# Kernel optimization log

Measured on AMD Instinct MI355X. Metric: run time of the kernel, lower is better.

The kernel has to match this reference:

```python
import jax, jax.numpy as jnp
import numpy as np

B, D, H, W, K = 32, 64, 32, 32, 8192
BETA, EMA_DECAY, EMA_EPS = 0.25, 0.99, 1e-05


def setup_inputs() -> dict:
    key = jax.random.key(0)
    k1, k2 = jax.random.split(key, 2)
    z = jax.random.normal(k1, (B, D, H, W), dtype=jnp.float32)
    embedding = jax.random.normal(k2, (K, D), dtype=jnp.float32)  # weight.data.normal_()
    ema_cluster_size = jnp.zeros((K,), dtype=jnp.float32)
    ema_embedding_avg = embedding  # initialized as clone of weights
    return {
        "z": z,
        "embedding": embedding,
        "ema_cluster_size": ema_cluster_size,
        "ema_embedding_avg": ema_embedding_avg,
    }


def reference(z, embedding, ema_cluster_size, ema_embedding_avg):
    b, d, h, w = z.shape
    k = embedding.shape[0]
    n = b * h * w

    # (b d h w) -> (b h w) d
    z_flat = jnp.transpose(z, (0, 2, 3, 1)).reshape(n, d)

    # squared L2 distances: ||z||^2 + ||e||^2 - 2 z e^T   -> [n, k]
    distances = (
        jnp.sum(z_flat * z_flat, axis=1, keepdims=True)
        + jnp.sum(embedding * embedding, axis=1)
        - 2.0 * jnp.einsum("nd,kd->nk", z_flat, embedding)
    )
    encoding_indices = jnp.argmin(distances, axis=1)  # [n]

    # codebook gather
    z_q_flat = embedding[encoding_indices]  # [n, d]
    z_quantized = jnp.transpose(z_q_flat.reshape(b, h, w, d), (0, 3, 1, 2))

    # commitment loss (encoder loss; quantized is detached in original)
    loss = BETA * jnp.mean((jax.lax.stop_gradient(z_quantized) - z) ** 2)

    # perplexity from one-hot mean (computed via scatter-add instead of dense one-hot)
    counts = jnp.zeros((k,), dtype=jnp.float32).at[encoding_indices].add(1.0)  # [k]
    enc_mean = counts / n
    perplexity = jnp.exp(-jnp.sum(enc_mean * jnp.log(enc_mean + 1e-10)))

    # EMA codebook update (training path)
    batch_cluster_size = counts
    batch_embedding_avg = jnp.zeros((k, d), dtype=z_flat.dtype).at[encoding_indices].add(z_flat)
    new_cluster_size = EMA_DECAY * ema_cluster_size + (1.0 - EMA_DECAY) * batch_cluster_size
    new_embedding_avg = EMA_DECAY * ema_embedding_avg + (1.0 - EMA_DECAY) * batch_embedding_avg
    new_embedding = new_embedding_avg / (new_cluster_size + EMA_EPS)[:, None]

    # straight-through estimator
    z_quantized_st = z + jax.lax.stop_gradient(z_quantized - z)

    return (
        z_quantized_st,
        loss,
        perplexity,
        encoding_indices,
        new_embedding,
        new_cluster_size,
        new_embedding_avg,
    )
```

## Files before the change

kernel.cpp:

```cpp
#include <hip/hip_runtime.h>
#include <math.h>

#define KCL   8192
#define DIM   64
#define NPTS  32768
#define HW    1024
#define PLANE 65536

__global__ __launch_bounds__(256) void e2_kernel(const float* __restrict__ emb,
                                                 float* __restrict__ e2) {
    int k = blockIdx.x * 256 + threadIdx.x;
    const float4* row = (const float4*)(emb + (size_t)k * DIM);
    float s = 0.f;
#pragma unroll
    for (int i = 0; i < DIM / 4; ++i) {
        float4 v = row[i];
        s += v.x * v.x + v.y * v.y + v.z * v.z + v.w * v.w;
    }
    e2[k] = s;
}

__global__ __launch_bounds__(256) void vq_main(
    const float* __restrict__ z, const float* __restrict__ emb,
    const float* __restrict__ e2g, float* __restrict__ counts,
    float* __restrict__ bavg, float* __restrict__ loss_ws,
    float* __restrict__ zq_out, float* __restrict__ idx_out) {
    __shared__ float z_lds[64 * 68];
    __shared__ float e_lds[64 * 68];
    __shared__ float e2_lds[64];

    const int t   = threadIdx.x;
    const int pg  = t >> 4;
    const int cg  = t & 15;
    const int p0  = blockIdx.x * 64;
    const int b   = p0 >> 10;
    const int hw0 = p0 & 1023;
    const float* zb = z + (size_t)b * PLANE + hw0;

    {
        int seg = t & 15, d0 = t >> 4;
#pragma unroll
        for (int r = 0; r < 4; ++r) {
            int d = d0 + 16 * r;
            float4 v = *(const float4*)(zb + d * HW + 4 * seg);
            *(float4*)&z_lds[d * 68 + 4 * seg] = v;
        }
    }

    float best[4];
    int   bestk[4];
#pragma unroll
    for (int i = 0; i < 4; ++i) { best[i] = 3.4e38f; bestk[i] = 0; }

    for (int k0 = 0; k0 < KCL; k0 += 64) {
        __syncthreads();
        {
            int c = t >> 2, s0 = t & 3;
#pragma unroll
            for (int r = 0; r < 4; ++r) {
                int seg = s0 + 4 * r;
                float4 v = *(const float4*)(emb + (size_t)(k0 + c) * DIM + 4 * seg);
                e_lds[(4 * seg + 0) * 68 + c] = v.x;
                e_lds[(4 * seg + 1) * 68 + c] = v.y;
                e_lds[(4 * seg + 2) * 68 + c] = v.z;
                e_lds[(4 * seg + 3) * 68 + c] = v.w;
            }
            if (t < 64) e2_lds[t] = e2g[k0 + t];
        }
        __syncthreads();

        float acc[4][4];
#pragma unroll
        for (int i = 0; i < 4; ++i)
#pragma unroll
            for (int j = 0; j < 4; ++j) acc[i][j] = 0.f;

#pragma unroll 4
        for (int d = 0; d < 64; ++d) {
            float4 zv = *(const float4*)&z_lds[d * 68 + 4 * pg];
            float4 ev = *(const float4*)&e_lds[d * 68 + 4 * cg];
            acc[0][0] += zv.x * ev.x; acc[0][1] += zv.x * ev.y;
            acc[0][2] += zv.x * ev.z; acc[0][3] += zv.x * ev.w;
            acc[1][0] += zv.y * ev.x; acc[1][1] += zv.y * ev.y;
            acc[1][2] += zv.y * ev.z; acc[1][3] += zv.y * ev.w;
            acc[2][0] += zv.z * ev.x; acc[2][1] += zv.z * ev.y;
            acc[2][2] += zv.z * ev.z; acc[2][3] += zv.z * ev.w;
            acc[3][0] += zv.w * ev.x; acc[3][1] += zv.w * ev.y;
            acc[3][2] += zv.w * ev.z; acc[3][3] += zv.w * ev.w;
        }

#pragma unroll
        for (int i = 0; i < 4; ++i) {
#pragma unroll
            for (int j = 0; j < 4; ++j) {
                float dist = e2_lds[4 * cg + j] - 2.f * acc[i][j];
                int   kk   = k0 + 4 * cg + j;
                if (dist < best[i]) { best[i] = dist; bestk[i] = kk; }
            }
        }
    }

#pragma unroll
    for (int i = 0; i < 4; ++i) {
        float bd = best[i];
        int   bk = bestk[i];
        for (int off = 8; off > 0; off >>= 1) {
            float od = __shfl_xor(bd, off, 16);
            int   ok = __shfl_xor(bk, off, 16);
            if (od < bd || (od == bd && ok < bk)) { bd = od; bk = ok; }
        }
        best[i] = bd; bestk[i] = bk;
    }

    __syncthreads();
    float* zq_lds = e_lds;

    float lsum = 0.f;
#pragma unroll
    for (int j = 0; j < 4; ++j) {
        int k = bestk[j];
        int p = 4 * pg + j;
        float4 ev = *(const float4*)(emb + (size_t)k * DIM + 4 * cg);
        float zv0 = z_lds[(4 * cg + 0) * 68 + p];
        float zv1 = z_lds[(4 * cg + 1) * 68 + p];
        float zv2 = z_lds[(4 * cg + 2) * 68 + p];
        float zv3 = z_lds[(4 * cg + 3) * 68 + p];
        zq_lds[(4 * cg + 0) * 68 + p] = ev.x;
        zq_lds[(4 * cg + 1) * 68 + p] = ev.y;
        zq_lds[(4 * cg + 2) * 68 + p] = ev.z;
        zq_lds[(4 * cg + 3) * 68 + p] = ev.w;
        float d0 = ev.x - zv0, d1 = ev.y - zv1, d2 = ev.z - zv2, d3 = ev.w - zv3;
        lsum += d0 * d0 + d1 * d1 + d2 * d2 + d3 * d3;
        atomicAdd(&bavg[(size_t)k * DIM + 4 * cg + 0], zv0);
        atomicAdd(&bavg[(size_t)k * DIM + 4 * cg + 1], zv1);
        atomicAdd(&bavg[(size_t)k * DIM + 4 * cg + 2], zv2);
        atomicAdd(&bavg[(size_t)k * DIM + 4 * cg + 3], zv3);
        if (cg == 0) {
            atomicAdd(&counts[k], 1.0f);
            idx_out[p0 + p] = (float)k;
        }
    }

#pragma unroll
    for (int off = 32; off > 0; off >>= 1) lsum += __shfl_xor(lsum, off, 64);
    if ((t & 63) == 0) atomicAdd(loss_ws, lsum);

    __syncthreads();
    {
        int seg = t & 15, d0 = t >> 4;
#pragma unroll
        for (int r = 0; r < 4; ++r) {
            int d = d0 + 16 * r;
            float4 q = *(const float4*)&zq_lds[d * 68 + 4 * seg];
            *(float4*)(zq_out + (size_t)b * PLANE + d * HW + hw0 + 4 * seg) = q;
        }
    }
}

__global__ __launch_bounds__(256) void ema_kernel(
    const float* __restrict__ ema_cs, const float* __restrict__ ema_avg,
    const float* __restrict__ counts, const float* __restrict__ bavg,
    float* __restrict__ out_ncs, float* __restrict__ out_navg,
    float* __restrict__ out_nemb) {
    int tid = blockIdx.x * 256 + threadIdx.x;
    int k = tid >> 4;
    float ncs = 0.99f * ema_cs[k] + 0.01f * counts[k];
    float den = ncs + 1e-5f;
    float4 ea = ((const float4*)ema_avg)[tid];
    float4 ba = ((const float4*)bavg)[tid];
    float4 na, ne;
    na.x = 0.99f * ea.x + 0.01f * ba.x;
    na.y = 0.99f * ea.y + 0.01f * ba.y;
    na.z = 0.99f * ea.z + 0.01f * ba.z;
    na.w = 0.99f * ea.w + 0.01f * ba.w;
    ne.x = na.x / den; ne.y = na.y / den; ne.z = na.z / den; ne.w = na.w / den;
    ((float4*)out_navg)[tid] = na;
    ((float4*)out_nemb)[tid] = ne;
    if ((tid & 15) == 0) out_ncs[k] = ncs;
}

__global__ __launch_bounds__(256) void scalars_kernel(
    const float* __restrict__ counts, const float* __restrict__ loss_ws,
    float* __restrict__ out_loss, float* __restrict__ out_perp) {
    __shared__ float red[4];
    float s = 0.f;
    for (int k = threadIdx.x; k < KCL; k += 256) {
        float p = counts[k] * (1.0f / (float)NPTS);
        s += p * logf(p + 1e-10f);
    }
#pragma unroll
    for (int off = 32; off > 0; off >>= 1) s += __shfl_xor(s, off, 64);
    if ((threadIdx.x & 63) == 0) red[threadIdx.x >> 6] = s;
    __syncthreads();
    if (threadIdx.x == 0) {
        float tot = red[0] + red[1] + red[2] + red[3];
        out_perp[0] = expf(-tot);
        out_loss[0] = 0.25f * loss_ws[0] / (float)(NPTS * DIM);
    }
}

extern "C" void kernel_launch(void* const* d_in, const int* in_sizes, int n_in,
                              void* d_out, int out_size, void* d_ws, size_t ws_size,
                              hipStream_t stream) {
    (void)in_sizes; (void)n_in; (void)out_size; (void)ws_size;
    const float* z       = (const float*)d_in[0];
    const float* emb     = (const float*)d_in[1];
    const float* ema_cs  = (const float*)d_in[2];
    const float* ema_avg = (const float*)d_in[3];

    float* out0      = (float*)d_out;
    float* out_loss  = out0 + 2097152;
    float* out_perp  = out_loss + 1;
    float* out_idx   = out_perp + 1;
    float* out_nemb  = out_idx + NPTS;
    float* out_ncs   = out_nemb + KCL * DIM;
    float* out_navg  = out_ncs + KCL;

    float* e2_ws     = (float*)d_ws;
    float* counts_ws = e2_ws + KCL;
    float* bavg_ws   = counts_ws + KCL;
    float* loss_ws   = bavg_ws + KCL * DIM;

    hipMemsetAsync((void*)counts_ws, 0, (size_t)(KCL + KCL * DIM + 1) * sizeof(float), stream);

    e2_kernel<<<KCL / 256, 256, 0, stream>>>(emb, e2_ws);
    vq_main<<<NPTS / 64, 256, 0, stream>>>(z, emb, e2_ws, counts_ws, bavg_ws,
                                           loss_ws, out0, out_idx);
    ema_kernel<<<KCL * DIM / 4 / 256, 256, 0, stream>>>(ema_cs, ema_avg, counts_ws,
                                                        bavg_ws, out_ncs, out_navg, out_nemb);
    scalars_kernel<<<1, 256, 0, stream>>>(counts_ws, loss_ws, out_loss, out_perp);
}
```

Before: 610.6 us.

## Restructure VQ distance loop with double-buffered codebook chunks and wave-level argmin

Reworks the main VQ kernel so each wave owns 16 points, with z read directly from global memory (wave-uniform, cached) and codebook chunks of 128 entries held in a swizzled, double-buffered LDS. The next chunk is prefetched into registers while the current one is computed, leaving one barrier per chunk. Each lane covers 2 codes by 16 points, and the argmin reduces across the full wave. The epilogue is rewritten to gather from global memory per point, and launch bounds request 2 blocks per CU. The risks are higher register pressure from 32 accumulators plus prefetch registers, and repeated global z loads inside the inner loop.

Result: slower. 884.5 us (+44.9%).

```diff
diff --git a/kernel.cpp b/kernel.cpp
--- a/kernel.cpp
+++ b/kernel.cpp
@@ -6,6 +6,10 @@
 #define NPTS  32768
 #define HW    1024
 #define PLANE 65536
+#define CCH   128
+#define NCH   (KCL/CCH)
+#define TP    16
+#define TC    2
 
 __global__ __launch_bounds__(256) void e2_kernel(const float* __restrict__ emb,
                                                  float* __restrict__ e2) {
@@ -20,140 +24,147 @@
     e2[k] = s;
 }
 
-__global__ __launch_bounds__(256) void vq_main(
+#define FMA4(zz, ib) \
+    acc[ib+0][0]=fmaf(zz.x,e0,acc[ib+0][0]); acc[ib+0][1]=fmaf(zz.x,e1,acc[ib+0][1]); \
+    acc[ib+1][0]=fmaf(zz.y,e0,acc[ib+1][0]); acc[ib+1][1]=fmaf(zz.y,e1,acc[ib+1][1]); \
+    acc[ib+2][0]=fmaf(zz.z,e0,acc[ib+2][0]); acc[ib+2][1]=fmaf(zz.z,e1,acc[ib+2][1]); \
+    acc[ib+3][0]=fmaf(zz.w,e0,acc[ib+3][0]); acc[ib+3][1]=fmaf(zz.w,e1,acc[ib+3][1]);
+
+__global__ __launch_bounds__(256, 2) void vq_main(
     const float* __restrict__ z, const float* __restrict__ emb,
     const float* __restrict__ e2g, float* __restrict__ counts,
     float* __restrict__ bavg, float* __restrict__ loss_ws,
     float* __restrict__ zq_out, float* __restrict__ idx_out) {
-    __shared__ float z_lds[64 * 68];
-    __shared__ float e_lds[64 * 68];
-    __shared__ float e2_lds[64];
-
-    const int t   = threadIdx.x;
-    const int pg  = t >> 4;
-    const int cg  = t & 15;
-    const int p0  = blockIdx.x * 64;
-    const int b   = p0 >> 10;
-    const int hw0 = p0 & 1023;
-    const float* zb = z + (size_t)b * PLANE + hw0;
+
+    __shared__ __align__(16) float ebuf[2][CCH * DIM];
+    __shared__ float e2buf[2][CCH];
+    __shared__ int   kbest_lds[64];
+
+    const int t    = threadIdx.x;
+    const int lane = t & 63;
+    const int wuni = __builtin_amdgcn_readfirstlane(t >> 6);
+    const int p0   = blockIdx.x * 64;
+    const int b    = p0 >> 10;
+    const int hw0  = p0 & 1023;
+
+    const float* zw = z + (size_t)b * PLANE + hw0 + 16 * wuni;
+
+    const int srow  = t >> 1;
+    const int sbase = (t & 1) * 8;
+    const int skey  = (t >> 3) & 15;
+    const int rb0 = (2 * lane) * DIM;
+    const int rb1 = rb0 + DIM;
+    const int sw4 = ((lane >> 1) & 15) << 2;
 
     {
-        int seg = t & 15, d0 = t >> 4;
-#pragma unroll
-        for (int r = 0; r < 4; ++r) {
-            int d = d0 + 16 * r;
-            float4 v = *(const float4*)(zb + d * HW + 4 * seg);
-            *(float4*)&z_lds[d * 68 + 4 * seg] = v;
-        }
-    }
-
-    float best[4];
-    int   bestk[4];
-#pragma unroll
-    for (int i = 0; i < 4; ++i) { best[i] = 3.4e38f; bestk[i] = 0; }
-
-    for (int k0 = 0; k0 < KCL; k0 += 64) {
-        __syncthreads();
-        {
-            int c = t >> 2, s0 = t & 3;
-#pragma unroll
-            for (int r = 0; r < 4; ++r) {
-                int seg = s0 + 4 * r;
-                float4 v = *(const float4*)(emb + (size_t)(k0 + c) * DIM + 4 * seg);
-                e_lds[(4 * seg + 0) * 68 + c] = v.x;
-                e_lds[(4 * seg + 1) * 68 + c] = v.y;
-                e_lds[(4 * seg + 2) * 68 + c] = v.z;
-                e_lds[(4 * seg + 3) * 68 + c] = v.w;
+        const float* src = emb + (size_t)srow * DIM;
+#pragma unroll
+        for (int i = 0; i < 8; ++i) {
+            int slot = sbase + i;
+            float4 v = *(const float4*)(src + slot * 4);
+            *(float4*)&ebuf[0][srow * DIM + ((slot ^ skey) << 2)] = v;
+        }
+        e2buf[0][t & 127] = e2g[t & 127];
+    }
+
+    float best[TP]; int bestk[TP];
+#pragma unroll
+    for (int i = 0; i < TP; ++i) { best[i] = 3.4e38f; bestk[i] = 0; }
+
+    __syncthreads();
+
+    for (int kc = 0; kc < NCH; ++kc) {
+        const int cur = kc & 1;
+        const int k0  = kc * CCH;
+
+        float4 st[8]; float e2st = 0.f;
+        const bool more = (kc + 1 < NCH);
+        if (more) {
+            const float* src = emb + (size_t)(k0 + CCH + srow) * DIM;
+#pragma unroll
+            for (int i = 0; i < 8; ++i) st[i] = *(const float4*)(src + (sbase + i) * 4);
+            e2st = e2g[k0 + CCH + (t & 127)];
+        }
+
+        float acc[TP][TC];
+#pragma unroll
+        for (int i = 0; i < TP; ++i) { acc[i][0] = 0.f; acc[i][1] = 0.f; }
+
+        const float* eb = &ebuf[cur][0];
+#pragma unroll 4
+        for (int dg = 0; dg < 16; ++dg) {
+            float4 ea = *(const float4*)&eb[rb0 + ((dg << 2) ^ sw4)];
+            float4 ec = *(const float4*)&eb[rb1 + ((dg << 2) ^ sw4)];
+#pragma unroll
+            for (int dd = 0; dd < 4; ++dd) {
+                const float* zd = zw + (size_t)(4 * dg + dd) * HW;
+                float4 z0 = *(const float4*)(zd);
+                float4 z1 = *(const float4*)(zd + 4);
+                float4 z2 = *(const float4*)(zd + 8);
+                float4 z3 = *(const float4*)(zd + 12);
+                float e0 = (dd == 0) ? ea.x : (dd == 1) ? ea.y : (dd == 2) ? ea.z : ea.w;
+                float e1 = (dd == 0) ? ec.x : (dd == 1) ? ec.y : (dd == 2) ? ec.z : ec.w;
+                FMA4(z0, 0) FMA4(z1, 4) FMA4(z2, 8) FMA4(z3, 12)
             }
-            if (t < 64) e2_lds[t] = e2g[k0 + t];
-        }
-        __syncthreads();
-
-        float acc[4][4];
-#pragma unroll
-        for (int i = 0; i < 4; ++i)
-#pragma unroll
-            for (int j = 0; j < 4; ++j) acc[i][j] = 0.f;
-
-#pragma unroll 4
-        for (int d = 0; d < 64; ++d) {
-            float4 zv = *(const float4*)&z_lds[d * 68 + 4 * pg];
-            float4 ev = *(const float4*)&e_lds[d * 68 + 4 * cg];
-            acc[0][0] += zv.x * ev.x; acc[0][1] += zv.x * ev.y;
-            acc[0][2] += zv.x * ev.z; acc[0][3] += zv.x * ev.w;
-            acc[1][0] += zv.y * ev.x; acc[1][1] += zv.y * ev.y;
-            acc[1][2] += zv.y * ev.z; acc[1][3] += zv.y * ev.w;
-            acc[2][0] += zv.z * ev.x; acc[2][1] += zv.z * ev.y;
-            acc[2][2] += zv.z * ev.z; acc[2][3] += zv.z * ev.w;
-            acc[3][0] += zv.w * ev.x; acc[3][1] += zv.w * ev.y;
-            acc[3][2] += zv.w * ev.z; acc[3][3] += zv.w * ev.w;
-        }
-
-#pragma unroll
-        for (int i = 0; i < 4; ++i) {
-#pragma unroll
-            for (int j = 0; j < 4; ++j) {
-                float dist = e2_lds[4 * cg + j] - 2.f * acc[i][j];
-                int   kk   = k0 + 4 * cg + j;
+        }
+
+#pragma unroll
+        for (int i = 0; i < TP; ++i) {
+#pragma unroll
+            for (int j = 0; j < TC; ++j) {
+                float dist = fmaf(-2.f, acc[i][j], e2buf[cur][2 * lane + j]);
+                int kk = k0 + 2 * lane + j;
                 if (dist < best[i]) { best[i] = dist; bestk[i] = kk; }
             }
         }
-    }
-
-#pragma unroll
-    for (int i = 0; i < 4; ++i) {
-        float bd = best[i];
-        int   bk = bestk[i];
-        for (int off = 8; off > 0; off >>= 1) {
-            float od = __shfl_xor(bd, off, 16);
-            int   ok = __shfl_xor(bk, off, 16);
+
+        if (more) {
+#pragma unroll
+            for (int i = 0; i < 8; ++i) {
+                int slot = sbase + i;
+                *(float4*)&ebuf[cur ^ 1][srow * DIM + ((slot ^ skey) << 2)] = st[i];
+            }
+            e2buf[cur ^ 1][t & 127] = e2st;
+        }
+        __syncthreads();
+    }
+
+#pragma unroll
+    for (int i = 0; i < TP; ++i) {
+        float bd = best[i]; int bk = bestk[i];
+#pragma unroll
+        for (int off = 32; off > 0; off >>= 1) {
+            float od = __shfl_xor(bd, off);
+            int   ok = __shfl_xor(bk, off);
             if (od < bd || (od == bd && ok < bk)) { bd = od; bk = ok; }
         }
-        best[i] = bd; bestk[i] = bk;
-    }
-
+        if (lane == 0) {
+            int p = 16 * wuni + i;
+            kbest_lds[p] = bk;
+            idx_out[p0 + p] = (float)bk;
+            atomicAdd(&counts[bk], 1.0f);
+        }
+    }
     __syncthreads();
-    float* zq_lds = e_lds;
-
-    float lsum = 0.f;
-#pragma unroll
-    for (int j = 0; j < 4; ++j) {
-        int k = bestk[j];
-        int p = 4 * pg + j;
-        float4 ev = *(const float4*)(emb + (size_t)k * DIM + 4 * cg);
-        float zv0 = z_lds[(4 * cg + 0) * 68 + p];
-        float zv1 = z_lds[(4 * cg + 1) * 68 + p];
-        float zv2 = z_lds[(4 * cg + 2) * 68 + p];
-        float zv3 = z_lds[(4 * cg + 3) * 68 + p];
-        zq_lds[(4 * cg + 0) * 68 + p] = ev.x;
-        zq_lds[(4 * cg + 1) * 68 + p] = ev.y;
-        zq_lds[(4 * cg + 2) * 68 + p] = ev.z;
-        zq_lds[(4 * cg + 3) * 68 + p] = ev.w;
-        float d0 = ev.x - zv0, d1 = ev.y - zv1, d2 = ev.z - zv2, d3 = ev.w - zv3;
-        lsum += d0 * d0 + d1 * d1 + d2 * d2 + d3 * d3;
-        atomicAdd(&bavg[(size_t)k * DIM + 4 * cg + 0], zv0);
-        atomicAdd(&bavg[(size_t)k * DIM + 4 * cg + 1], zv1);
-        atomicAdd(&bavg[(size_t)k * DIM + 4 * cg + 2], zv2);
-        atomicAdd(&bavg[(size_t)k * DIM + 4 * cg + 3], zv3);
-        if (cg == 0) {
-            atomicAdd(&counts[k], 1.0f);
-            idx_out[p0 + p] = (float)k;
-        }
-    }
-
-#pragma unroll
-    for (int off = 32; off > 0; off >>= 1) lsum += __shfl_xor(lsum, off, 64);
-    if ((t & 63) == 0) atomicAdd(loss_ws, lsum);
-
-    __syncthreads();
+
     {
-        int seg = t & 15, d0 = t >> 4;
-#pragma unroll
-        for (int r = 0; r < 4; ++r) {
-            int d = d0 + 16 * r;
-            float4 q = *(const float4*)&zq_lds[d * 68 + 4 * seg];
-            *(float4*)(zq_out + (size_t)b * PLANE + d * HW + hw0 + 4 * seg) = q;
-        }
+        const int p = t & 63, q = t >> 6;
+        const int k = kbest_lds[p];
+        const float* er = emb + (size_t)k * DIM;
+        float lsum = 0.f;
+#pragma unroll
+        for (int dd = 0; dd < 16; ++dd) {
+            int d = 16 * q + dd;
+            size_t gidx = (size_t)b * PLANE + (size_t)d * HW + hw0 + p;
+            float zv = z[gidx];
+            float ev = er[d];
+            zq_out[gidx] = ev;
+            float df = ev - zv; lsum += df * df;
+            atomicAdd(&bavg[(size_t)k * DIM + d], zv);
+        }
+#pragma unroll
+        for (int off = 32; off > 0; off >>= 1) lsum += __shfl_xor(lsum, off);
+        if (lane == 0) atomicAdd(loss_ws, lsum);
     }
 }
 
```

## Split codebook search across blocks with per-thread point registers and a merge kernel

Applied to the files above, without the earlier changes.

Replaces the LDS-tiled 64x64 register-blocked distance kernel with a split-K scheme. Each thread holds one point's 64-dim vector in registers and scans one eighth of the codebook, reading embedding rows as wave-uniform broadcast loads. A separate merge kernel picks the best of the 8 partial results, then does the gather, loss and EMA atomics, using the new-embedding output buffer as scratch. This drops the per-tile syncthreads and LDS traffic, but each embedding load now feeds only one FMA per thread, so the kernel depends on scalar-cache broadcast throughput. Ties across splits now go to the lower split, which still gives the first index.

Measured after the change: 932.4 us. 52.7% more time.

```diff
diff --git a/kernel.cpp b/kernel.cpp
--- a/kernel.cpp
+++ b/kernel.cpp
@@ -1,11 +1,13 @@
 #include <hip/hip_runtime.h>
 #include <math.h>
 
-#define KCL   8192
-#define DIM   64
-#define NPTS  32768
-#define HW    1024
-#define PLANE 65536
+#define KCL    8192
+#define DIM    64
+#define NPTS   32768
+#define HW     1024
+#define PLANE  65536
+#define SPLITS 8
+#define CBLK   (KCL / SPLITS)
 
 __global__ __launch_bounds__(256) void e2_kernel(const float* __restrict__ emb,
                                                  float* __restrict__ e2) {
@@ -20,141 +22,71 @@
     e2[k] = s;
 }
 
-__global__ __launch_bounds__(256) void vq_main(
+__global__ __launch_bounds__(256) void vq_dist(
     const float* __restrict__ z, const float* __restrict__ emb,
-    const float* __restrict__ e2g, float* __restrict__ counts,
-    float* __restrict__ bavg, float* __restrict__ loss_ws,
-    float* __restrict__ zq_out, float* __restrict__ idx_out) {
-    __shared__ float z_lds[64 * 68];
-    __shared__ float e_lds[64 * 68];
-    __shared__ float e2_lds[64];
+    const float* __restrict__ e2g, float* __restrict__ bestO,
+    int* __restrict__ kbestO) {
+    const int t  = threadIdx.x;
+    const int ks = blockIdx.x & (SPLITS - 1);
+    const int pb = blockIdx.x >> 3;
+    const int p  = (pb << 8) + t;
+    const int b  = p >> 10, hw = p & 1023;
+    const float* zp = z + (size_t)b * PLANE + hw;
 
-    const int t   = threadIdx.x;
-    const int pg  = t >> 4;
-    const int cg  = t & 15;
-    const int p0  = blockIdx.x * 64;
-    const int b   = p0 >> 10;
-    const int hw0 = p0 & 1023;
-    const float* zb = z + (size_t)b * PLANE + hw0;
+    float zv[DIM];
+#pragma unroll
+    for (int d = 0; d < DIM; ++d) zv[d] = zp[(size_t)d * HW];
 
-    {
-        int seg = t & 15, d0 = t >> 4;
+    float best = 3.4e38f;
+    int   bk   = 0;
+    const int k0 = ks * CBLK;
+    for (int k = k0; k < k0 + CBLK; ++k) {
+        const float* __restrict__ er = emb + ((size_t)k << 6);
+        float acc = 0.f;
 #pragma unroll
-        for (int r = 0; r < 4; ++r) {
-            int d = d0 + 16 * r;
-            float4 v = *(const float4*)(zb + d * HW + 4 * seg);
-            *(float4*)&z_lds[d * 68 + 4 * seg] = v;
-        }
+        for (int d = 0; d < DIM; ++d) acc = fmaf(er[d], zv[d], acc);
+        float dist = fmaf(-2.f, acc, e2g[k]);
+        if (dist < best) { best = dist; bk = k; }
     }
+    bestO[ks * NPTS + p]  = best;
+    kbestO[ks * NPTS + p] = bk;
+}
 
-    float best[4];
-    int   bestk[4];
+__global__ __launch_bounds__(256) void merge_epi(
+    const float* __restrict__ z, const float* __restrict__ emb,
+    const float* __restrict__ bestO, const int* __restrict__ kbestO,
+    float* __restrict__ counts, float* __restrict__ bavg,
+    float* __restrict__ loss_ws, float* __restrict__ zq_out,
+    float* __restrict__ idx_out) {
+    const int t = threadIdx.x;
+    const int p = blockIdx.x * 256 + t;
+    float best = 3.4e38f;
+    int   bk   = 0;
 #pragma unroll
-    for (int i = 0; i < 4; ++i) { best[i] = 3.4e38f; bestk[i] = 0; }
+    for (int s = 0; s < SPLITS; ++s) {
+        float d = bestO[s * NPTS + p];
+        int   k = kbestO[s * NPTS + p];
+        if (d < best) { best = d; bk = k; }
+    }
+    idx_out[p] = (float)bk;
+    atomicAdd(&counts[bk], 1.0f);
 
-    for (int k0 = 0; k0 < KCL; k0 += 64) {
-        __syncthreads();
-        {
-            int c = t >> 2, s0 = t & 3;
-#pragma unroll
-            for (int r = 0; r < 4; ++r) {
-                int seg = s0 + 4 * r;
-                float4 v = *(const float4*)(emb + (size_t)(k0 + c) * DIM + 4 * seg);
-                e_lds[(4 * seg + 0) * 68 + c] = v.x;
-                e_lds[(4 * seg + 1) * 68 + c] = v.y;
-                e_lds[(4 * seg + 2) * 68 + c] = v.z;
-                e_lds[(4 * seg + 3) * 68 + c] = v.w;
-            }
-            if (t < 64) e2_lds[t] = e2g[k0 + t];
-        }
-        __syncthreads();
-
-        float acc[4][4];
-#pragma unroll
-        for (int i = 0; i < 4; ++i)
-#pragma unroll
-            for (int j = 0; j < 4; ++j) acc[i][j] = 0.f;
-
-#pragma unroll 4
-        for (int d = 0; d < 64; ++d) {
-            float4 zv = *(const float4*)&z_lds[d * 68 + 4 * pg];
-            float4 ev = *(const float4*)&e_lds[d * 68 + 4 * cg];
-            acc[0][0] += zv.x * ev.x; acc[0][1] += zv.x * ev.y;
-            acc[0][2] += zv.x * ev.z; acc[0][3] += zv.x * ev.w;
-            acc[1][0] += zv.y * ev.x; acc[1][1] += zv.y * ev.y;
-            acc[1][2] += zv.y * ev.z; acc[1][3] += zv.y * ev.w;
-            acc[2][0] += zv.z * ev.x; acc[2][1] += zv.z * ev.y;
-            acc[2][2] += zv.z * ev.z; acc[2][3] += zv.z * ev.w;
-            acc[3][0] += zv.w * ev.x; acc[3][1] += zv.w * ev.y;
-            acc[3][2] += zv.w * ev.z; acc[3][3] += zv.w * ev.w;
-        }
-
-#pragma unroll
-        for (int i = 0; i < 4; ++i) {
-#pragma unroll
-            for (int j = 0; j < 4; ++j) {
-                float dist = e2_lds[4 * cg + j] - 2.f * acc[i][j];
-                int   kk   = k0 + 4 * cg + j;
-                if (dist < best[i]) { best[i] = dist; bestk[i] = kk; }
-            }
-        }
-    }
-
-#pragma unroll
-    for (int i = 0; i < 4; ++i) {
-        float bd = best[i];
-        int   bk = bestk[i];
-        for (int off = 8; off > 0; off >>= 1) {
-            float od = __shfl_xor(bd, off, 16);
-            int   ok = __shfl_xor(bk, off, 16);
-            if (od < bd || (od == bd && ok < bk)) { bd = od; bk = ok; }
-        }
-        best[i] = bd; bestk[i] = bk;
-    }
-
-    __syncthreads();
-    float* zq_lds = e_lds;
-
+    const int b = p >> 10, hw = p & 1023;
+    const float* er = emb + ((size_t)bk << 6);
     float lsum = 0.f;
 #pragma unroll
-    for (int j = 0; j < 4; ++j) {
-        int k = bestk[j];
-        int p = 4 * pg + j;
-        float4 ev = *(const float4*)(emb + (size_t)k * DIM + 4 * cg);
-        float zv0 = z_lds[(4 * cg + 0) * 68 + p];
-        float zv1 = z_lds[(4 * cg + 1) * 68 + p];
-        float zv2 = z_lds[(4 * cg + 2) * 68 + p];
-        float zv3 = z_lds[(4 * cg + 3) * 68 + p];
-        zq_lds[(4 * cg + 0) * 68 + p] = ev.x;
-        zq_lds[(4 * cg + 1) * 68 + p] = ev.y;
-        zq_lds[(4 * cg + 2) * 68 + p] = ev.z;
-        zq_lds[(4 * cg + 3) * 68 + p] = ev.w;
-        float d0 = ev.x - zv0, d1 = ev.y - zv1, d2 = ev.z - zv2, d3 = ev.w - zv3;
-        lsum += d0 * d0 + d1 * d1 + d2 * d2 + d3 * d3;
-        atomicAdd(&bavg[(size_t)k * DIM + 4 * cg + 0], zv0);
-        atomicAdd(&bavg[(size_t)k * DIM + 4 * cg + 1], zv1);
-        atomicAdd(&bavg[(size_t)k * DIM + 4 * cg + 2], zv2);
-        atomicAdd(&bavg[(size_t)k * DIM + 4 * cg + 3], zv3);
-        if (cg == 0) {
-            atomicAdd(&counts[k], 1.0f);
-            idx_out[p0 + p] = (float)k;
-        }
+    for (int d = 0; d < DIM; ++d) {
+        size_t g  = (size_t)b * PLANE + (size_t)d * HW + hw;
+        float zvv = z[g];
+        float ev  = er[d];
+        zq_out[g] = ev;
+        float df  = ev - zvv;
+        lsum = fmaf(df, df, lsum);
+        atomicAdd(&bavg[((size_t)bk << 6) + d], zvv);
     }
-
 #pragma unroll
-    for (int off = 32; off > 0; off >>= 1) lsum += __shfl_xor(lsum, off, 64);
+    for (int off = 32; off > 0; off >>= 1) lsum += __shfl_xor(lsum, off);
     if ((t & 63) == 0) atomicAdd(loss_ws, lsum);
-
-    __syncthreads();
-    {
-        int seg = t & 15, d0 = t >> 4;
-#pragma unroll
-        for (int r = 0; r < 4; ++r) {
-            int d = d0 + 16 * r;
-            float4 q = *(const float4*)&zq_lds[d * 68 + 4 * seg];
-            *(float4*)(zq_out + (size_t)b * PLANE + d * HW + hw0 + 4 * seg) = q;
-        }
-    }
 }
 
 __global__ __launch_bounds__(256) void ema_kernel(
@@ -221,11 +153,15 @@
     float* bavg_ws   = counts_ws + KCL;
     float* loss_ws   = bavg_ws + KCL * DIM;
 
+    float* bestO  = out_nemb;
+    int*   kbestO = (int*)(out_nemb + SPLITS * NPTS);
+
     hipMemsetAsync((void*)counts_ws, 0, (size_t)(KCL + KCL * DIM + 1) * sizeof(float), stream);
 
     e2_kernel<<<KCL / 256, 256, 0, stream>>>(emb, e2_ws);
-    vq_main<<<NPTS / 64, 256, 0, stream>>>(z, emb, e2_ws, counts_ws, bavg_ws,
-                                           loss_ws, out0, out_idx);
+    vq_dist<<<(NPTS / 256) * SPLITS, 256, 0, stream>>>(z, emb, e2_ws, bestO, kbestO);
+    merge_epi<<<NPTS / 256, 256, 0, stream>>>(z, emb, bestO, kbestO, counts_ws,
+                                              bavg_ws, loss_ws, out0, out_idx);
     ema_kernel<<<KCL * DIM / 4 / 256, 256, 0, stream>>>(ema_cs, ema_avg, counts_ws,
                                                         bavg_ws, out_ncs, out_navg, out_nemb);
     scalars_kernel<<<1, 256, 0, stream>>>(counts_ws, loss_ws, out_loss, out_perp);
```
